# Kernel optimization log

Hardware: AMD Instinct MI355X
Metric: run time of the kernel (lower is better)

Reference implementation:

```python
import jax, jax.numpy as jnp
import numpy as np

EMB = 1024
HEADS = 16
HD = EMB // HEADS
EPS = 1e-5

def _ln(x, g, b):
    m = jnp.mean(x, axis=-1, keepdims=True)
    v = jnp.mean((x - m) ** 2, axis=-1, keepdims=True)
    return (x - m) * jax.lax.rsqrt(v + EPS) * g + b

def setup_inputs() -> dict:
    key = jax.random.key(0)
    ks = jax.random.split(key, 12)
    s_in = 1.0 / np.sqrt(EMB)
    s_ff = 1.0 / np.sqrt(4 * EMB)
    return {
        "x": jax.random.normal(ks[0], (2, 2048, EMB), jnp.float32),
        "wq": jax.random.uniform(ks[1], (HEADS, EMB, HD), jnp.float32, -s_in, s_in),
        "wk": jax.random.uniform(ks[2], (HEADS, EMB, HD), jnp.float32, -s_in, s_in),
        "wv": jax.random.uniform(ks[3], (HEADS, EMB, HD), jnp.float32, -s_in, s_in),
        "wo": jax.random.uniform(ks[4], (EMB, EMB), jnp.float32, -s_in, s_in),
        "bo": jax.random.uniform(ks[5], (EMB,), jnp.float32, -s_in, s_in),
        "g1": jnp.ones((EMB,), jnp.float32),
        "b1": jnp.zeros((EMB,), jnp.float32),
        "g2": jnp.ones((EMB,), jnp.float32),
        "b2": jnp.zeros((EMB,), jnp.float32),
        "w1": jax.random.uniform(ks[6], (EMB, 4 * EMB), jnp.float32, -s_in, s_in),
        "bf1": jax.random.uniform(ks[7], (4 * EMB,), jnp.float32, -s_in, s_in),
        "w2": jax.random.uniform(ks[8], (4 * EMB, EMB), jnp.float32, -s_ff, s_ff),
        "bf2": jax.random.uniform(ks[9], (EMB,), jnp.float32, -s_ff, s_ff),
    }

def reference(x, wq, wk, wv, wo, bo, g1, b1, g2, b2, w1, bf1, w2, bf2):
    B, T, C = x.shape
    h = _ln(x, g1, b1)
    # all heads batched: [B,H,T,HD]
    q = jnp.einsum('btc,hcd->bhtd', h, wq)
    k = jnp.einsum('btc,hcd->bhtd', h, wk)
    v = jnp.einsum('btc,hcd->bhtd', h, wv)
    # NOTE: original scales by full emb_size C**-0.5, not head_size
    scores = jnp.einsum('bhtd,bhsd->bhts', q, k) * (C ** -0.5)
    causal = jnp.tril(jnp.ones((T, T), bool))
    scores = jnp.where(causal, scores, -jnp.inf)
    w = jax.nn.softmax(scores, axis=-1)
    attn = jnp.einsum('bhts,bhsd->bhtd', w, v)
    attn = attn.transpose(0, 2, 1, 3).reshape(B, T, C)  # concat heads
    x = x + attn @ wo + bo
    h2 = _ln(x, g2, b2)
    ffn = jax.nn.relu(h2 @ w1 + bf1) @ w2 + bf2
    return x + ffn
```

## Files before the change

### kernel.cpp

```cpp
#include <hip/hip_runtime.h>
#include <hip/hip_bf16.h>

typedef __bf16 bf16x8 __attribute__((ext_vector_type(8)));
typedef float f32x4 __attribute__((ext_vector_type(4)));
typedef short s16x8 __attribute__((ext_vector_type(8)));

#define DEV __device__ __forceinline__

DEV float b2f(unsigned short u) {
  unsigned int x = ((unsigned int)u) << 16;
  return __builtin_bit_cast(float, x);
}
DEV unsigned short f2b(float f) {
  unsigned int x = __builtin_bit_cast(unsigned int, f);
  x += 0x7fffu + ((x >> 16) & 1u);
  return (unsigned short)(x >> 16);
}
DEV unsigned int f2b2(float a, float b) {
  float2 t; t.x = a; t.y = b;
  __hip_bfloat162 v = __float22bfloat162_rn(t);
  unsigned int r;
  __builtin_memcpy(&r, &v, 4);
  return r;
}
DEV f32x4 mfma16(bf16x8 a, bf16x8 b, f32x4 c) {
  return __builtin_amdgcn_mfma_f32_16x16x32_bf16(a, b, c, 0, 0, 0);
}
DEV void gl2lds16(const unsigned short* g, unsigned short* l) {
  __builtin_amdgcn_global_load_lds(
      (const __attribute__((address_space(1))) void*)g,
      (__attribute__((address_space(3))) void*)l, 16, 0, 0);
}

__global__ __launch_bounds__(256)
void transpose_k(const float* __restrict__ in, unsigned short* __restrict__ out,
                 int K, int N, long zin, long zout) {
  __shared__ float tile[32][33];
  in  += (size_t)blockIdx.z * zin;
  out += (size_t)blockIdx.z * zout;
  int n0 = blockIdx.x * 32, k0 = blockIdx.y * 32;
  int tx = threadIdx.x, ty = threadIdx.y;
  #pragma unroll
  for (int i = ty; i < 32; i += 8)
    tile[i][tx] = in[(size_t)(k0 + i) * N + n0 + tx];
  __syncthreads();
  #pragma unroll
  for (int i = ty; i < 32; i += 8)
    out[(size_t)(n0 + i) * K + k0 + tx] = f2b(tile[tx][i]);
}

__global__ __launch_bounds__(256)
void transpose_qkv(const float* __restrict__ wq, const float* __restrict__ wk,
                   const float* __restrict__ wv, unsigned short* __restrict__ out) {
  __shared__ float tile[32][33];
  const int z = blockIdx.z;
  const float* in = (z < 16) ? (wq + (size_t)z * 65536)
                  : (z < 32) ? (wk + (size_t)(z - 16) * 65536)
                             : (wv + (size_t)(z - 32) * 65536);
  unsigned short* o = out + (size_t)z * 65536;
  int n0 = blockIdx.x * 32, k0 = blockIdx.y * 32;
  int tx = threadIdx.x, ty = threadIdx.y;
  #pragma unroll
  for (int i = ty; i < 32; i += 8)
    tile[i][tx] = in[(size_t)(k0 + i) * 64 + n0 + tx];
  __syncthreads();
  #pragma unroll
  for (int i = ty; i < 32; i += 8)
    o[(size_t)(n0 + i) * 1024 + k0 + tx] = f2b(tile[tx][i]);
}

__global__ __launch_bounds__(256)
void ln_kernel(const float* __restrict__ x, const float* __restrict__ g,
               const float* __restrict__ b, unsigned short* __restrict__ o) {
  __shared__ float rs[4];
  __shared__ float rq[4];
  int row = blockIdx.x, tid = threadIdx.x;
  const float* xr = x + (size_t)row * 1024;
  float4 raw = ((const float4*)xr)[tid];
  float s = raw.x + raw.y + raw.z + raw.w;
  float q = raw.x*raw.x + raw.y*raw.y + raw.z*raw.z + raw.w*raw.w;
  #pragma unroll
  for (int off = 32; off > 0; off >>= 1) {
    s += __shfl_down(s, off);
    q += __shfl_down(q, off);
  }
  int wave = tid >> 6;
  if ((tid & 63) == 0) { rs[wave] = s; rq[wave] = q; }
  __syncthreads();
  float ts = rs[0] + rs[1] + rs[2] + rs[3];
  float tq = rq[0] + rq[1] + rq[2] + rq[3];
  float mean = ts * (1.0f/1024.0f);
  float var = tq * (1.0f/1024.0f) - mean*mean;
  float rstd = rsqrtf(var + 1e-5f);
  float4 gr = ((const float4*)g)[tid];
  float4 br = ((const float4*)b)[tid];
  float o0 = (raw.x-mean)*rstd*gr.x + br.x;
  float o1 = (raw.y-mean)*rstd*gr.y + br.y;
  float o2 = (raw.z-mean)*rstd*gr.z + br.z;
  float o3 = (raw.w-mean)*rstd*gr.w + br.w;
  uint2 ov;
  ov.x = f2b2(o0, o1);
  ov.y = f2b2(o2, o3);
  ((uint2*)(o + (size_t)row * 1024))[tid] = ov;
}

template<bool RELU, bool BIAS, bool VFUSE>
__global__ __launch_bounds__(512, 2)
void gemm8p(const unsigned short* __restrict__ A, const unsigned short* __restrict__ Bt,
            const float* __restrict__ bias, void* __restrict__ Cv,
            unsigned short* __restrict__ vT, int NTn, int N, int K) {
  __shared__ unsigned short As[4][256*32];
  __shared__ unsigned short Bs[4][256*32];
  const int tid = threadIdx.x;
  const int lane = tid & 63, wave = tid >> 6;
  const int quad = lane >> 4, l16 = lane & 15;
  const int wm = wave >> 2, wn = wave & 3;
  const int nwg = gridDim.x;
  const int id = blockIdx.x;
  const int id2 = (id & 7) * (nwg >> 3) + (id >> 3);
  const int mt = id2 / NTn, nt = id2 % NTn;
  const int m0 = mt * 256, n0 = nt * 256;

  f32x4 acc[8][4];
  #pragma unroll
  for (int i = 0; i < 8; ++i)
    #pragma unroll
    for (int j = 0; j < 4; ++j) acc[i][j] = (f32x4){0.f, 0.f, 0.f, 0.f};

  const int srow = tid >> 2;
  const int scc  = (((tid & 3) ^ ((srow >> 1) & 3)) * 8);
  const unsigned short* Ab = A + (size_t)m0 * K;
  const unsigned short* Bb = Bt + (size_t)n0 * K;

  const int NT = K >> 5;
  const int H  = NT << 2;

  auto stage = [&](int h) {
    const int Tt = h >> 2, part = h & 3, kk = Tt << 5;
    const int buf = Tt & 3;
    if (part == 0)
      gl2lds16(Ab + (size_t)srow * K + kk + scc,         &As[buf][tid * 8]);
    else if (part == 1)
      gl2lds16(Ab + (size_t)(srow + 128) * K + kk + scc, &As[buf][4096 + tid * 8]);
    else if (part == 2)
      gl2lds16(Bb + (size_t)srow * K + kk + scc,         &Bs[buf][tid * 8]);
    else
      gl2lds16(Bb + (size_t)(srow + 128) * K + kk + scc, &Bs[buf][4096 + tid * 8]);
  };

  #pragma unroll
  for (int h = 0; h < 10; ++h) stage(h);
  asm volatile("s_waitcnt vmcnt(6)" ::: "memory");
  asm volatile("s_barrier" ::: "memory");

  const int qsw = (quad ^ ((l16 >> 1) & 3)) * 8;
  const int arow0 = wm * 128 + l16;
  const int brow0 = wn * 64 + l16;

  for (int T = 0; T < NT; ++T) {
    const int buf = T & 3;
    bf16x8 bq[4];
    {
      bf16x8 af[4];
      #pragma unroll
      for (int i = 0; i < 4; ++i)
        af[i] = __builtin_bit_cast(bf16x8,
          *(const s16x8*)&As[buf][(arow0 + i*16)*32 + qsw]);
      #pragma unroll
      for (int j = 0; j < 4; ++j)
        bq[j] = __builtin_bit_cast(bf16x8,
          *(const s16x8*)&Bs[buf][(brow0 + j*16)*32 + qsw]);
      const int h = 4*T + 10;
      if (h < H)     stage(h);
      if (h + 1 < H) stage(h + 1);
      asm volatile("s_barrier" ::: "memory");
      __builtin_amdgcn_s_setprio(1);
      #pragma unroll
      for (int i = 0; i < 4; ++i)
        #pragma unroll
        for (int j = 0; j < 4; ++j)
          acc[i][j] = mfma16(af[i], bq[j], acc[i][j]);
      __builtin_amdgcn_s_setprio(0);
      asm volatile("s_barrier" ::: "memory");
    }
    {
      bf16x8 af[4];
      #pragma unroll
      for (int i = 0; i < 4; ++i)
        af[i] = __builtin_bit_cast(bf16x8,
          *(const s16x8*)&As[buf][(arow0 + 64 + i*16)*32 + qsw]);
      const int h = 4*T + 12;
      if (h < H)     stage(h);
      if (h + 1 < H) stage(h + 1);
      if (T + 3 < NT)      { asm volatile("s_waitcnt vmcnt(6)" ::: "memory"); }
      else if (T + 2 < NT) { asm volatile("s_waitcnt vmcnt(4)" ::: "memory"); }
      else if (T + 1 < NT) { asm volatile("s_waitcnt vmcnt(0)" ::: "memory"); }
      asm volatile("s_barrier" ::: "memory");
      __builtin_amdgcn_s_setprio(1);
      #pragma unroll
      for (int i = 0; i < 4; ++i)
        #pragma unroll
        for (int j = 0; j < 4; ++j)
          acc[4 + i][j] = mfma16(af[i], bq[j], acc[4 + i][j]);
      __builtin_amdgcn_s_setprio(0);
      asm volatile("s_barrier" ::: "memory");
    }
  }

  #pragma unroll
  for (int ii = 0; ii < 8; ++ii) {
    const int row = m0 + wm*128 + ii*16 + quad*4;
    #pragma unroll
    for (int j = 0; j < 4; ++j) {
      const int col = n0 + wn*64 + j*16 + l16;
      if (VFUSE && col >= 2048) {
        const int b = row >> 11, tloc = row & 2047;
        const int h = (col - 2048) >> 6, d = col & 63;
        ushort4 pk;
        pk.x = f2b(acc[ii][j][0]);
        pk.y = f2b(acc[ii][j][1]);
        pk.z = f2b(acc[ii][j][2]);
        pk.w = f2b(acc[ii][j][3]);
        *(ushort4*)&vT[((size_t)((b*16 + h)*64 + d))*2048 + tloc] = pk;
      } else {
        float bv = BIAS ? bias[col] : 0.f;
        #pragma unroll
        for (int r = 0; r < 4; ++r) {
          float v = acc[ii][j][r] + bv;
          if (RELU) v = fmaxf(v, 0.f);
          ((unsigned short*)Cv)[(size_t)(row + r) * N + col] = f2b(v);
        }
      }
    }
  }
}

__global__ __launch_bounds__(256)
void gemm_n1024(const unsigned short* __restrict__ A, const unsigned short* __restrict__ Bt,
                const float* __restrict__ bias, const float* __restrict__ resid,
                float* __restrict__ C, int M, int N, int K) {
  __shared__ unsigned short As[3][64*64];
  __shared__ unsigned short Bs[3][128*64];
  const int tid = threadIdx.x;
  const int lane = tid & 63;
  const int quad = lane >> 4, l16 = lane & 15;
  const int wave = tid >> 6;
  const int id = blockIdx.x;
  const int xcd = id & 7, i2 = id >> 3;
  const int mt = (xcd << 3) | (i2 >> 3);
  const int nt = i2 & 7;
  const int m0 = mt * 64, n0 = nt * 128;
  const int wm = (wave >> 1) * 32, wn = (wave & 1) * 64;

  f32x4 acc[2][4];
  #pragma unroll
  for (int i = 0; i < 2; ++i)
    #pragma unroll
    for (int j = 0; j < 4; ++j) acc[i][j] = (f32x4){0.f, 0.f, 0.f, 0.f};

  const int srow = tid >> 3;
  const int scc  = ((tid & 7) ^ (srow & 7)) * 8;
  const unsigned short* Ab = A + (size_t)m0 * K;
  const unsigned short* Bb = Bt + (size_t)n0 * K;

  auto stage = [&](int buf, int k0) {
    unsigned short* Ad = &As[buf][0];
    unsigned short* Bd = &Bs[buf][0];
    gl2lds16(Ab + (size_t)srow * K + k0 + scc,         Ad + tid * 8);
    gl2lds16(Ab + (size_t)(srow + 32) * K + k0 + scc,  Ad + 2048 + tid * 8);
    gl2lds16(Bb + (size_t)srow * K + k0 + scc,         Bd + tid * 8);
    gl2lds16(Bb + (size_t)(srow + 32) * K + k0 + scc,  Bd + 2048 + tid * 8);
    gl2lds16(Bb + (size_t)(srow + 64) * K + k0 + scc,  Bd + 4096 + tid * 8);
    gl2lds16(Bb + (size_t)(srow + 96) * K + k0 + scc,  Bd + 6144 + tid * 8);
  };

  const int niter = K >> 6;
  stage(0, 0);
  stage(1, 64);

  int bufc = 0;
  for (int it = 0; it < niter; ++it) {
    if (it + 1 < niter) {
      asm volatile("s_waitcnt vmcnt(6)" ::: "memory");
    } else {
      asm volatile("s_waitcnt vmcnt(0)" ::: "memory");
    }
    __builtin_amdgcn_s_barrier();
    if (it + 2 < niter) {
      int bufn = bufc + 2; if (bufn >= 3) bufn -= 3;
      stage(bufn, (it + 2) * 64);
    }
    const unsigned short* Ar = &As[bufc][0];
    const unsigned short* Br = &Bs[bufc][0];
    #pragma unroll
    for (int s = 0; s < 2; ++s) {
      bf16x8 af[2], bfr[4];
      #pragma unroll
      for (int i = 0; i < 2; ++i) {
        const int R = wm + i*16 + l16;
        af[i] = __builtin_bit_cast(bf16x8,
          *(const s16x8*)&Ar[R*64 + (((s*4 + quad) ^ (R & 7)) * 8)]);
      }
      #pragma unroll
      for (int j = 0; j < 4; ++j) {
        const int R = wn + j*16 + l16;
        bfr[j] = __builtin_bit_cast(bf16x8,
          *(const s16x8*)&Br[R*64 + (((s*4 + quad) ^ (R & 7)) * 8)]);
      }
      #pragma unroll
      for (int i = 0; i < 2; ++i)
        #pragma unroll
        for (int j = 0; j < 4; ++j)
          acc[i][j] = mfma16(af[i], bfr[j], acc[i][j]);
    }
    bufc = (bufc == 2) ? 0 : bufc + 1;
  }

  #pragma unroll
  for (int i = 0; i < 2; ++i) {
    const int row = m0 + wm + i*16 + quad*4;
    #pragma unroll
    for (int j = 0; j < 4; ++j) {
      const int col = n0 + wn + j*16 + l16;
      const float bv = bias[col];
      #pragma unroll
      for (int r = 0; r < 4; ++r)
        C[(size_t)(row + r) * N + col] = acc[i][j][r] + bv + resid[(size_t)(row + r) * N + col];
    }
  }
}

__global__ __launch_bounds__(256)
void attn_kernel(const unsigned short* __restrict__ qkv,
                 const unsigned short* __restrict__ vT,
                 unsigned short* __restrict__ outc) {
  __shared__ unsigned short Ks[2][64*64];
  __shared__ unsigned short Vs[2][64*64];
  __shared__ unsigned short Ps[4*16*72];
  const int tid = threadIdx.x, lane = tid & 63, wave = tid >> 6;
  const int quad = lane >> 4, l16 = lane & 15;
  const int bh = blockIdx.y, b = bh >> 4, h = bh & 15;
  const int jA = blockIdx.x, jB = 31 - jA;
  const size_t tokbase = (size_t)b * 2048 * 3072;
  const unsigned short* Q  = qkv + tokbase + h * 64;
  const unsigned short* Kg = qkv + tokbase + 1024 + h * 64;
  const unsigned short* Vg = vT + (size_t)bh * 64 * 2048;

  const s16x8 ones_s = {0x3F80, 0x3F80, 0x3F80, 0x3F80, 0x3F80, 0x3F80, 0x3F80, 0x3F80};
  const bf16x8 onesf = __builtin_bit_cast(bf16x8, ones_s);

  bf16x8 qf[2][2];
  #pragma unroll
  for (int t = 0; t < 2; ++t) {
    const int qrow = (t ? jB : jA) * 64 + wave * 16 + l16;
    #pragma unroll
    for (int s = 0; s < 2; ++s) {
      s16x8 raw = *(const s16x8*)(Q + (size_t)qrow * 3072 + s * 32 + quad * 8);
      unsigned short* rp = (unsigned short*)&raw;
      #pragma unroll
      for (int j = 0; j < 8; ++j) rp[j] = f2b(b2f(rp[j]) * 0.03125f);
      qf[t][s] = __builtin_bit_cast(bf16x8, raw);
    }
  }

  f32x4 accO[2][4];
  f32x4 accS[2] = {(f32x4){0.f,0.f,0.f,0.f}, (f32x4){0.f,0.f,0.f,0.f}};
  #pragma unroll
  for (int t = 0; t < 2; ++t)
    #pragma unroll
    for (int i = 0; i < 4; ++i) accO[t][i] = (f32x4){0.f, 0.f, 0.f, 0.f};

  const int r8 = lane >> 3;
  const int cs = (((lane & 7) ^ r8) * 8);

  auto stage = [&](int buf, int kv0) {
    #pragma unroll
    for (int i = 0; i < 2; ++i) {
      int row = wave * 16 + i * 8;
      gl2lds16(Kg + (size_t)(kv0 + row + r8) * 3072 + cs, &Ks[buf][row * 64 + lane * 8]);
      gl2lds16(Vg + (size_t)(row + r8) * 2048 + kv0 + cs, &Vs[buf][row * 64 + lane * 8]);
    }
  };

  const int ntile = jB + 1;
  stage(0, 0);
  __syncthreads();

  for (int it = 0; it < ntile; ++it) {
    const int buf = it & 1;
    if (it + 1 < ntile) stage(buf ^ 1, (it + 1) * 64);

    #pragma unroll
    for (int t = 0; t < 2; ++t) {
      const int jT = t ? jB : jA;
      if (it > jT) continue;
      f32x4 sv[4];
      #pragma unroll
      for (int ni = 0; ni < 4; ++ni) {
        sv[ni] = (f32x4){0.f, 0.f, 0.f, 0.f};
        #pragma unroll
        for (int s = 0; s < 2; ++s) {
          bf16x8 kf = __builtin_bit_cast(bf16x8,
            *(const s16x8*)&Ks[buf][(ni*16 + l16)*64 + (((s*4 + quad) ^ (l16 & 7)) * 8)]);
          sv[ni] = mfma16(qf[t][s], kf, sv[ni]);
        }
      }
      if (it == jT) {
        const int rowg = jT*64 + wave*16 + quad*4;
        const int kv0 = it * 64;
        #pragma unroll
        for (int ni = 0; ni < 4; ++ni) {
          const int colg = kv0 + ni*16 + l16;
          #pragma unroll
          for (int r = 0; r < 4; ++r)
            if (colg > rowg + r) sv[ni][r] = -__builtin_inff();
        }
      }
      #pragma unroll
      for (int ni = 0; ni < 4; ++ni) {
        float p0 = __expf(sv[ni][0]);
        float p1 = __expf(sv[ni][1]);
        float p2 = __expf(sv[ni][2]);
        float p3 = __expf(sv[ni][3]);
        unsigned int u01 = f2b2(p0, p1);
        unsigned int u23 = f2b2(p2, p3);
        const int base = wave*1152 + ni*16 + l16;
        Ps[base + (quad*4 + 0)*72] = (unsigned short)u01;
        Ps[base + (quad*4 + 1)*72] = (unsigned short)(u01 >> 16);
        Ps[base + (quad*4 + 2)*72] = (unsigned short)u23;
        Ps[base + (quad*4 + 3)*72] = (unsigned short)(u23 >> 16);
      }
      __asm__ volatile("s_waitcnt lgkmcnt(0)" ::: "memory");
      #pragma unroll
      for (int s = 0; s < 2; ++s) {
        bf16x8 pf = __builtin_bit_cast(bf16x8,
          *(const s16x8*)&Ps[wave*1152 + l16*72 + s*32 + quad*8]);
        accS[t] = mfma16(pf, onesf, accS[t]);
        #pragma unroll
        for (int ni = 0; ni < 4; ++ni) {
          bf16x8 vf = __builtin_bit_cast(bf16x8,
            *(const s16x8*)&Vs[buf][(ni*16 + l16)*64 + (((s*4 + quad) ^ (l16 & 7)) * 8)]);
          accO[t][ni] = mfma16(pf, vf, accO[t][ni]);
        }
      }
    }
    __syncthreads();
  }

  #pragma unroll
  for (int t = 0; t < 2; ++t) {
    const int rowg = (t ? jB : jA)*64 + wave*16 + quad*4;
    float inv[4];
    #pragma unroll
    for (int r = 0; r < 4; ++r) inv[r] = __builtin_amdgcn_rcpf(accS[t][r]);
    #pragma unroll
    for (int ni = 0; ni < 4; ++ni)
      #pragma unroll
      for (int r = 0; r < 4; ++r)
        outc[(size_t)(b*2048 + rowg + r) * 1024 + h*64 + ni*16 + l16]
          = f2b(accO[t][ni][r] * inv[r]);
  }
}

extern "C" void kernel_launch(void* const* d_in, const int* in_sizes, int n_in,
                              void* d_out, int out_size, void* d_ws, size_t ws_size,
                              hipStream_t stream) {
  (void)in_sizes; (void)n_in; (void)out_size; (void)ws_size;
  const float* x   = (const float*)d_in[0];
  const float* wq  = (const float*)d_in[1];
  const float* wk  = (const float*)d_in[2];
  const float* wv  = (const float*)d_in[3];
  const float* wo  = (const float*)d_in[4];
  const float* bo  = (const float*)d_in[5];
  const float* g1  = (const float*)d_in[6];
  const float* b1  = (const float*)d_in[7];
  const float* g2  = (const float*)d_in[8];
  const float* b2  = (const float*)d_in[9];
  const float* w1  = (const float*)d_in[10];
  const float* bf1 = (const float*)d_in[11];
  const float* w2  = (const float*)d_in[12];
  const float* bf2 = (const float*)d_in[13];
  float* out = (float*)d_out;

  unsigned short* ws    = (unsigned short*)d_ws;
  unsigned short* wqkvt = ws;
  unsigned short* wot   = wqkvt + 3*1024*1024;
  unsigned short* w1t   = wot   + 1024*1024;
  unsigned short* w2t   = w1t   + 4096*1024;
  unsigned short* hbuf  = w2t   + 4096*1024;
  unsigned short* qkvb  = hbuf  + 4096*1024;
  unsigned short* attnb = qkvb  + (size_t)4096*3072;
  float*          x2b   = (float*)(attnb + 4096*1024);
  unsigned short* vTb   = (unsigned short*)x2b;
  unsigned short* midb  = qkvb;

  dim3 tb(32, 8);
  transpose_qkv<<<dim3(2,32,48), tb, 0, stream>>>(wq, wk, wv, wqkvt);
  transpose_k<<<dim3(32,32,1),  tb, 0, stream>>>(wo, wot, 1024, 1024, 0, 0);
  transpose_k<<<dim3(128,32,1), tb, 0, stream>>>(w1, w1t, 1024, 4096, 0, 0);
  transpose_k<<<dim3(32,128,1), tb, 0, stream>>>(w2, w2t, 4096, 1024, 0, 0);

  ln_kernel<<<4096, 256, 0, stream>>>(x, g1, b1, hbuf);
  gemm8p<false,false,true><<<192, 512, 0, stream>>>(
      hbuf, wqkvt, nullptr, qkvb, vTb, 12, 3072, 1024);
  attn_kernel<<<dim3(16,32), 256, 0, stream>>>(qkvb, vTb, attnb);
  gemm_n1024<<<512, 256, 0, stream>>>(attnb, wot, bo, x, x2b, 4096, 1024, 1024);
  ln_kernel<<<4096, 256, 0, stream>>>(x2b, g2, b2, hbuf);
  gemm8p<true,true,false><<<256, 512, 0, stream>>>(
      hbuf, w1t, bf1, midb, nullptr, 16, 4096, 1024);
  gemm_n1024<<<512, 256, 0, stream>>>(midb, w2t, bf2, x2b, out, 4096, 1024, 4096);
}
```

Baseline: 343.5 us.

## Use 128x128 tiles with intra-block split-K for N=1024 GEMMs

Result: faster. 325.8 us (-5.1%).

```diff
diff --git a/kernel.cpp b/kernel.cpp
--- a/kernel.cpp
+++ b/kernel.cpp
@@ -235,26 +235,27 @@
   }
 }
 
-__global__ __launch_bounds__(256)
-void gemm_n1024(const unsigned short* __restrict__ A, const unsigned short* __restrict__ Bt,
-                const float* __restrict__ bias, const float* __restrict__ resid,
-                float* __restrict__ C, int M, int N, int K) {
-  __shared__ unsigned short As[3][64*64];
-  __shared__ unsigned short Bs[3][128*64];
+__global__ __launch_bounds__(512)
+void gemm_t128(const unsigned short* __restrict__ A, const unsigned short* __restrict__ Bt,
+               const float* __restrict__ bias, const float* __restrict__ resid,
+               float* __restrict__ C, int M, int N, int K) {
+  __shared__ unsigned short SMEM[6*128*64];
   const int tid = threadIdx.x;
   const int lane = tid & 63;
   const int quad = lane >> 4, l16 = lane & 15;
   const int wave = tid >> 6;
+  const int sub = wave >> 2;
+  const int wq = wave & 3;
+  const int wm = (wq >> 1) * 64, wn = (wq & 1) * 64;
   const int id = blockIdx.x;
   const int xcd = id & 7, i2 = id >> 3;
-  const int mt = (xcd << 3) | (i2 >> 3);
+  const int mt = (xcd << 2) | (i2 >> 3);
   const int nt = i2 & 7;
-  const int m0 = mt * 64, n0 = nt * 128;
-  const int wm = (wave >> 1) * 32, wn = (wave & 1) * 64;
-
-  f32x4 acc[2][4];
-  #pragma unroll
-  for (int i = 0; i < 2; ++i)
+  const int m0 = mt * 128, n0 = nt * 128;
+
+  f32x4 acc[4][4];
+  #pragma unroll
+  for (int i = 0; i < 4; ++i)
     #pragma unroll
     for (int j = 0; j < 4; ++j) acc[i][j] = (f32x4){0.f, 0.f, 0.f, 0.f};
 
@@ -264,24 +265,23 @@
   const unsigned short* Bb = Bt + (size_t)n0 * K;
 
   auto stage = [&](int buf, int k0) {
-    unsigned short* Ad = &As[buf][0];
-    unsigned short* Bd = &Bs[buf][0];
-    gl2lds16(Ab + (size_t)srow * K + k0 + scc,         Ad + tid * 8);
-    gl2lds16(Ab + (size_t)(srow + 32) * K + k0 + scc,  Ad + 2048 + tid * 8);
-    gl2lds16(Bb + (size_t)srow * K + k0 + scc,         Bd + tid * 8);
-    gl2lds16(Bb + (size_t)(srow + 32) * K + k0 + scc,  Bd + 2048 + tid * 8);
-    gl2lds16(Bb + (size_t)(srow + 64) * K + k0 + scc,  Bd + 4096 + tid * 8);
-    gl2lds16(Bb + (size_t)(srow + 96) * K + k0 + scc,  Bd + 6144 + tid * 8);
+    unsigned short* Ad = SMEM + buf * 8192;
+    unsigned short* Bd = SMEM + 24576 + buf * 8192;
+    gl2lds16(Ab + (size_t)srow * K + k0 + scc,        Ad + tid * 8);
+    gl2lds16(Ab + (size_t)(srow + 64) * K + k0 + scc, Ad + 4096 + tid * 8);
+    gl2lds16(Bb + (size_t)srow * K + k0 + scc,        Bd + tid * 8);
+    gl2lds16(Bb + (size_t)(srow + 64) * K + k0 + scc, Bd + 4096 + tid * 8);
   };
 
   const int niter = K >> 6;
   stage(0, 0);
   stage(1, 64);
 
+  const int cc = sub * 4 + quad;
   int bufc = 0;
   for (int it = 0; it < niter; ++it) {
     if (it + 1 < niter) {
-      asm volatile("s_waitcnt vmcnt(6)" ::: "memory");
+      asm volatile("s_waitcnt vmcnt(4)" ::: "memory");
     } else {
       asm volatile("s_waitcnt vmcnt(0)" ::: "memory");
     }
@@ -290,42 +290,54 @@
       int bufn = bufc + 2; if (bufn >= 3) bufn -= 3;
       stage(bufn, (it + 2) * 64);
     }
-    const unsigned short* Ar = &As[bufc][0];
-    const unsigned short* Br = &Bs[bufc][0];
-    #pragma unroll
-    for (int s = 0; s < 2; ++s) {
-      bf16x8 af[2], bfr[4];
-      #pragma unroll
-      for (int i = 0; i < 2; ++i) {
-        const int R = wm + i*16 + l16;
-        af[i] = __builtin_bit_cast(bf16x8,
-          *(const s16x8*)&Ar[R*64 + (((s*4 + quad) ^ (R & 7)) * 8)]);
-      }
-      #pragma unroll
-      for (int j = 0; j < 4; ++j) {
-        const int R = wn + j*16 + l16;
-        bfr[j] = __builtin_bit_cast(bf16x8,
-          *(const s16x8*)&Br[R*64 + (((s*4 + quad) ^ (R & 7)) * 8)]);
-      }
-      #pragma unroll
-      for (int i = 0; i < 2; ++i)
-        #pragma unroll
-        for (int j = 0; j < 4; ++j)
-          acc[i][j] = mfma16(af[i], bfr[j], acc[i][j]);
-    }
+    const unsigned short* Ar = SMEM + bufc * 8192;
+    const unsigned short* Br = SMEM + 24576 + bufc * 8192;
+    bf16x8 af[4], bfr[4];
+    #pragma unroll
+    for (int i = 0; i < 4; ++i) {
+      const int R = wm + i*16 + l16;
+      af[i] = __builtin_bit_cast(bf16x8,
+        *(const s16x8*)&Ar[R*64 + ((cc ^ (R & 7)) * 8)]);
+    }
+    #pragma unroll
+    for (int j = 0; j < 4; ++j) {
+      const int R = wn + j*16 + l16;
+      bfr[j] = __builtin_bit_cast(bf16x8,
+        *(const s16x8*)&Br[R*64 + ((cc ^ (R & 7)) * 8)]);
+    }
+    #pragma unroll
+    for (int i = 0; i < 4; ++i)
+      #pragma unroll
+      for (int j = 0; j < 4; ++j)
+        acc[i][j] = mfma16(af[i], bfr[j], acc[i][j]);
     bufc = (bufc == 2) ? 0 : bufc + 1;
   }
 
-  #pragma unroll
-  for (int i = 0; i < 2; ++i) {
+  __syncthreads();
+  float* ex = (float*)&SMEM[0];
+  float* w = ex + wq * 4096;
+  if (sub == 1) {
+    #pragma unroll
+    for (int i = 0; i < 4; ++i)
+      #pragma unroll
+      for (int j = 0; j < 4; ++j)
+        *(f32x4*)&w[(i*4 + j)*256 + lane*4] = acc[i][j];
+  }
+  __syncthreads();
+  if (sub == 1) return;
+
+  #pragma unroll
+  for (int i = 0; i < 4; ++i) {
     const int row = m0 + wm + i*16 + quad*4;
     #pragma unroll
     for (int j = 0; j < 4; ++j) {
+      f32x4 oth = *(const f32x4*)&w[(i*4 + j)*256 + lane*4];
       const int col = n0 + wn + j*16 + l16;
       const float bv = bias[col];
       #pragma unroll
       for (int r = 0; r < 4; ++r)
-        C[(size_t)(row + r) * N + col] = acc[i][j][r] + bv + resid[(size_t)(row + r) * N + col];
+        C[(size_t)(row + r) * N + col] =
+            acc[i][j][r] + oth[r] + bv + resid[(size_t)(row + r) * N + col];
     }
   }
 }
@@ -504,9 +516,9 @@
   gemm8p<false,false,true><<<192, 512, 0, stream>>>(
       hbuf, wqkvt, nullptr, qkvb, vTb, 12, 3072, 1024);
   attn_kernel<<<dim3(16,32), 256, 0, stream>>>(qkvb, vTb, attnb);
-  gemm_n1024<<<512, 256, 0, stream>>>(attnb, wot, bo, x, x2b, 4096, 1024, 1024);
+  gemm_t128<<<256, 512, 0, stream>>>(attnb, wot, bo, x, x2b, 4096, 1024, 1024);
   ln_kernel<<<4096, 256, 0, stream>>>(x2b, g2, b2, hbuf);
   gemm8p<true,true,false><<<256, 512, 0, stream>>>(
       hbuf, w1t, bf1, midb, nullptr, 16, 4096, 1024);
-  gemm_n1024<<<512, 256, 0, stream>>>(midb, w2t, bf2, x2b, out, 4096, 1024, 4096);
-}
+  gemm_t128<<<256, 512, 0, stream>>>(midb, w2t, bf2, x2b, out, 4096, 1024, 4096);
+}
```
